# Optimization experiments

Hardware: AMD Instinct MI355X
Metric: run time of the kernel (lower is better)

## Reference

```python
import jax, jax.numpy as jnp
import numpy as np

N_NODES = 50000
N_EDGES = 500000
F_DIM = 128
N_REL = 8
N_LAYERS = 2
NEG_SLOPE = 0.2  # PyG RGATConv default negative_slope


def setup_inputs() -> dict:
    key = jax.random.key(0)
    ks = jax.random.split(key, 6)
    x = jax.random.normal(ks[0], (N_NODES, F_DIM), dtype=jnp.float32)
    edge_index = jax.random.randint(ks[1], (2, N_EDGES), 0, N_NODES)
    edge_type = jax.random.randint(ks[2], (N_EDGES,), 0, N_REL)
    # Per-layer relation weights [L, R, F_in, F_out], attention vectors q,k [L, F_out, 1], bias [L, F_out]
    W = jax.random.normal(ks[3], (N_LAYERS, N_REL, F_DIM, F_DIM), dtype=jnp.float32) * (1.0 / np.sqrt(F_DIM)).astype(np.float32)
    att_q = jax.random.normal(ks[4], (N_LAYERS, F_DIM, 1), dtype=jnp.float32) * 0.1
    att_k = jax.random.normal(ks[5], (N_LAYERS, F_DIM, 1), dtype=jnp.float32) * 0.1
    bias = jnp.zeros((N_LAYERS, F_DIM), dtype=jnp.float32)
    return {"x": x, "W": W, "att_q": att_q, "att_k": att_k, "bias": bias,
            "edge_index": edge_index, "edge_type": edge_type}


def _segment_softmax(logits, seg, num_segments):
    # Numerically stable softmax over edges grouped by destination node.
    m = jax.ops.segment_max(logits, seg, num_segments=num_segments)
    m = jax.lax.stop_gradient(m)
    e = jnp.exp(logits - m[seg])
    denom = jax.ops.segment_sum(e, seg, num_segments=num_segments)
    return e / (denom[seg] + 1e-16)


def _rgat_layer(h, src, dst, edge_type, W, q, k, b):
    # h: [N, F]; W: [R, F, F]. Project once per relation, then gather per edge
    # (avoids materializing [E, F, F] per-edge weight gathers).
    n = h.shape[0]
    xw = jnp.einsum('nf,rfg->rng', h, W)          # [R, N, F]
    out_j = xw[edge_type, src]                    # [E, F] transformed source feats
    out_i = xw[edge_type, dst]                    # [E, F] transformed dest feats
    # additive self-attention: leaky_relu(q(x_i) + k(x_j)), heads=1, dim=1
    logits = jax.nn.leaky_relu((out_i @ q + out_j @ k)[:, 0], NEG_SLOPE)  # [E]
    alpha = _segment_softmax(logits, dst, n)      # across-relation softmax per dst node
    agg = jax.ops.segment_sum(alpha[:, None] * out_j, dst, num_segments=n)  # [N, F]
    return agg + b


def reference(x, W, att_q, att_k, bias, edge_index, edge_type):
    src, dst = edge_index[0], edge_index[1]
    h = x
    for l in range(W.shape[0]):  # small fixed layer count
        h = _rgat_layer(h, src, dst, edge_type, W[l], att_q[l], att_k[l], bias[l])
        h = jax.nn.relu(h)  # dropout is identity in eval mode
    return h
```

## Files before the change

kernel.cpp:

```cpp
#include <hip/hip_runtime.h>
#include <hip/hip_bf16.h>
#include <hip/hip_fp16.h>

#define N_NODES 50000
#define N_EDGES 500000
#define F_DIM   128
#define N_REL   8
#define N_LAYERS 2
#define NEG_SLOPE 0.2f

#define NBLK_N ((N_NODES + 255) / 256)

typedef _Float16 half8 __attribute__((ext_vector_type(8)));
typedef float f32x4  __attribute__((ext_vector_type(4)));


__device__ inline float lrelu(float l) { return (l > 0.f) ? l : NEG_SLOPE * l; }

__global__ __launch_bounds__(256) void prep_h(const float* __restrict__ H,
                                              _Float16* __restrict__ Hf) {
    const size_t i8 = (size_t)blockIdx.x * 256 + threadIdx.x;
    if (i8 >= (size_t)N_NODES * F_DIM / 8) return;
    const float* src = H + i8 * 8;
    float av[8];
    *(float4*)(av)     = *(const float4*)(src);
    *(float4*)(av + 4) = *(const float4*)(src + 4);
    alignas(16) _Float16 hb[8];
#pragma unroll
    for (int j = 0; j < 8; ++j) hb[j] = (_Float16)av[j];
    *(uint4*)(Hf + i8 * 8) = *(const uint4*)hb;
}

__global__ __launch_bounds__(256) void prep_w(const float* __restrict__ W,
                                              _Float16* __restrict__ Wf) {
    __shared__ float tile[64][F_DIM + 1];
    const int mat = blockIdx.x;
    const float* src = W + (size_t)mat * F_DIM * F_DIM;
    const int t = threadIdx.x;
    for (int hf = 0; hf < 2; ++hf) {
#pragma unroll
        for (int i = 0; i < 8; ++i) {
            int idx = t + i * 256;
            int f = idx >> 5, c4 = idx & 31;
            float4 v = *(const float4*)(src + (size_t)(hf * 64 + f) * F_DIM + c4 * 4);
            *(float4*)&tile[f][c4 * 4] = v;
        }
        __syncthreads();
        int g = t >> 1, fs = (t & 1) * 32;
        for (int c = 0; c < 4; ++c) {
            alignas(16) _Float16 th[8];
#pragma unroll
            for (int j = 0; j < 8; ++j) th[j] = (_Float16)tile[fs + c * 8 + j][g];
            size_t o = ((size_t)mat * F_DIM + g) * F_DIM + hf * 64 + fs + c * 8;
            *(uint4*)(Wf + o) = *(const uint4*)th;
        }
        __syncthreads();
    }
}

#define GBM 512
__global__ __launch_bounds__(256, 2) void gemm_xw(const _Float16* __restrict__ Hf,
                                                  const _Float16* __restrict__ Wf,
                                                  const float* __restrict__ qv_g,
                                                  const float* __restrict__ kv_g,
                                                  __half* __restrict__ xw,
                                                  float* __restrict__ a_q,
                                                  float* __restrict__ a_k) {
    __shared__ _Float16 lds[F_DIM * F_DIM];
    const int r   = blockIdx.y;
    const int tid = threadIdx.x;
    const int lane = tid & 63, w = tid >> 6;
    const int q = lane >> 4, ln = lane & 15;

    {
        const _Float16* src = Wf + (size_t)r * F_DIM * F_DIM;
#pragma unroll
        for (int i = 0; i < 8; ++i) {
            int chunk = tid + i * 256;
            int gg = chunk >> 4, c8 = chunk & 15;
            uint4 v = *(const uint4*)(src + gg * F_DIM + c8 * 8);
            *(uint4*)(lds + gg * F_DIM + ((c8 ^ (gg & 15)) * 8)) = v;
        }
    }

    float qvl[8], kvl[8];
#pragma unroll
    for (int t = 0; t < 8; ++t) {
        qvl[t] = qv_g[t * 16 + ln];
        kvl[t] = kv_g[t * 16 + ln];
    }

    __syncthreads();

    for (int t4 = 0; t4 < 4; ++t4) {
        const int rb0 = blockIdx.x * GBM + t4 * 128;
        if (rb0 >= N_NODES) break;

        half8 Af[2][4];
#pragma unroll
        for (int rt = 0; rt < 2; ++rt) {
            int row = rb0 + w * 32 + rt * 16 + ln;
            int ar = (row < N_NODES) ? row : (N_NODES - 1);
            const _Float16* hp = Hf + (size_t)ar * F_DIM;
#pragma unroll
            for (int ks = 0; ks < 4; ++ks)
                Af[rt][ks] = *(const half8*)(hp + ks * 32 + q * 8);
        }

        f32x4 acc[2][8];
#pragma unroll
        for (int rt = 0; rt < 2; ++rt)
#pragma unroll
            for (int t = 0; t < 8; ++t) acc[rt][t] = (f32x4)(0.f);

#pragma unroll
        for (int ks = 0; ks < 4; ++ks) {
            const int jx = (((ks * 4 + q) ^ ln)) << 3;
            half8 Bf[8];
#pragma unroll
            for (int c = 0; c < 8; ++c)
                Bf[c] = *(const half8*)(lds + (c * 16 + ln) * F_DIM + jx);
#pragma unroll
            for (int c = 0; c < 8; ++c)
#pragma unroll
                for (int rt = 0; rt < 2; ++rt)
                    acc[rt][c] = __builtin_amdgcn_mfma_f32_16x16x32_f16(Af[rt][ks], Bf[c], acc[rt][c], 0, 0, 0);
        }

#pragma unroll
        for (int rt = 0; rt < 2; ++rt) {
            float pq[4], pk[4];
#pragma unroll
            for (int reg = 0; reg < 4; ++reg) {
                const int row = rb0 + w * 32 + rt * 16 + q * 4 + reg;
                alignas(16) unsigned short hs[8];
                float sq = 0.f, sk = 0.f;
#pragma unroll
                for (int t = 0; t < 8; ++t) {
                    float v = acc[rt][t][reg];
                    __half hv = __float2half(v);
                    hs[t] = *reinterpret_cast<unsigned short*>(&hv);
                    sq = fmaf(v, qvl[t], sq);
                    sk = fmaf(v, kvl[t], sk);
                }
                if (row < N_NODES)
                    *(uint4*)(xw + ((size_t)r * N_NODES + row) * F_DIM + ln * 8) = *(const uint4*)hs;
                pq[reg] = sq; pk[reg] = sk;
            }
#pragma unroll
            for (int reg = 0; reg < 4; ++reg) {
#pragma unroll
                for (int m = 1; m <= 8; m <<= 1) {
                    pq[reg] += __shfl_xor(pq[reg], m);
                    pk[reg] += __shfl_xor(pk[reg], m);
                }
            }
            if (ln == 0) {
#pragma unroll
                for (int reg = 0; reg < 4; ++reg) {
                    const int row = rb0 + w * 32 + rt * 16 + q * 4 + reg;
                    if (row < N_NODES) {
                        a_q[r * N_NODES + row] = pq[reg];
                        a_k[r * N_NODES + row] = pk[reg];
                    }
                }
            }
        }
    }
}


__global__ __launch_bounds__(256) void count_kernel(const int* __restrict__ dstp,
                                                    int* __restrict__ cnt) {
    int e = blockIdx.x * 256 + threadIdx.x;
    if (e < N_EDGES) atomicAdd(cnt + dstp[e], 1);
}

__global__ __launch_bounds__(256) void block_sum_kernel(const int* __restrict__ cnt,
                                                        int* __restrict__ partial) {
    __shared__ int s[256];
    int idx = blockIdx.x * 256 + threadIdx.x;
    int v = (idx < N_NODES) ? cnt[idx] : 0;
    s[threadIdx.x] = v;
    __syncthreads();
    for (int off = 128; off > 0; off >>= 1) {
        if (threadIdx.x < off) s[threadIdx.x] += s[threadIdx.x + off];
        __syncthreads();
    }
    if (threadIdx.x == 0) partial[blockIdx.x] = s[0];
}

__global__ __launch_bounds__(256) void scan_partials_kernel(int* __restrict__ partial,
                                                            int* __restrict__ row_ptr) {
    __shared__ int s[256];
    int t = threadIdx.x;
    int v = (t < NBLK_N) ? partial[t] : 0;
    s[t] = v;
    __syncthreads();
#pragma unroll
    for (int off = 1; off < 256; off <<= 1) {
        int x = (t >= off) ? s[t - off] : 0;
        __syncthreads();
        s[t] += x;
        __syncthreads();
    }
    if (t < NBLK_N) partial[t] = s[t] - v;
    if (t == 0) row_ptr[N_NODES] = N_EDGES;
}

__global__ __launch_bounds__(256) void scan_block_kernel(const int* __restrict__ cnt,
                                                         const int* __restrict__ partial,
                                                         int* __restrict__ row_ptr) {
    __shared__ int s[256];
    int t = threadIdx.x;
    int idx = blockIdx.x * 256 + t;
    int v = (idx < N_NODES) ? cnt[idx] : 0;
    s[t] = v;
    __syncthreads();
#pragma unroll
    for (int off = 1; off < 256; off <<= 1) {
        int x = (t >= off) ? s[t - off] : 0;
        __syncthreads();
        s[t] += x;
        __syncthreads();
    }
    if (idx < N_NODES) row_ptr[idx] = partial[blockIdx.x] + s[t] - v;
}

__global__ __launch_bounds__(256) void scatter_kernel(const int* __restrict__ srcp,
                                                      const int* __restrict__ dstp,
                                                      const int* __restrict__ etp,
                                                      const int* __restrict__ row_ptr,
                                                      int* __restrict__ cursor,
                                                      unsigned* __restrict__ sorted,
                                                      unsigned short* __restrict__ dst16) {
    int e = blockIdx.x * 256 + threadIdx.x;
    if (e >= N_EDGES) return;
    int d = dstp[e];
    int pos = atomicAdd(cursor + d, 1);
    int j = row_ptr[d] + pos;
    sorted[j] = (unsigned)srcp[e] | ((unsigned)etp[e] << 16);
    dst16[j] = (unsigned short)d;
}

__global__ __launch_bounds__(256) void logits_kernel(const float* __restrict__ a_q,
                                                     const float* __restrict__ a_k,
                                                     const unsigned* __restrict__ sorted,
                                                     const unsigned short* __restrict__ dst16,
                                                     float* __restrict__ lgt) {
    int j = blockIdx.x * 256 + threadIdx.x;
    if (j >= N_EDGES) return;
    unsigned p = sorted[j];
    int s = p & 0xffff, t = p >> 16;
    int d = dst16[j];
    lgt[j] = lrelu(a_q[t * N_NODES + d] + a_k[t * N_NODES + s]);
}

__device__ inline void accum8(float* acc, uint4 v, float a) {
    const __half2* h2 = reinterpret_cast<const __half2*>(&v);
#pragma unroll
    for (int t = 0; t < 4; ++t) {
        float2 f = __half22float2(h2[t]);
        acc[t * 2]     = fmaf(a, f.x, acc[t * 2]);
        acc[t * 2 + 1] = fmaf(a, f.y, acc[t * 2 + 1]);
    }
}
__device__ inline const uint4* xwrow(const __half* xw, unsigned p, int ln) {
    return (const uint4*)(xw + (((size_t)(p >> 16)) * N_NODES + (p & 0xffff)) * F_DIM + ln * 8);
}

__global__ __launch_bounds__(256) void agg_fused(const __half* __restrict__ xw,
                                                 const float* __restrict__ lgt,
                                                 const int* __restrict__ row_ptr,
                                                 const unsigned* __restrict__ sorted,
                                                 const float* __restrict__ bias,
                                                 float* __restrict__ outp,
                                                 _Float16* __restrict__ hfp) {
    const int lane = threadIdx.x & 63;
    const int wave = threadIdx.x >> 6;
    const int half = lane >> 5, hl = lane & 31;
    const int d0 = blockIdx.x * 8 + wave * 2;
    if (d0 >= N_NODES) return;
    const int dmy = d0 + half;
    const int dv = (dmy < N_NODES) ? dmy : (N_NODES - 1);
    const int beg = row_ptr[dv], end = row_ptr[dv + 1];
    int cnt = (dmy < N_NODES) ? (end - beg) : 0;
    const int cntO = __shfl_xor(cnt, 32);
    const int cmax = (cnt > cntO) ? cnt : cntO;

    if (cmax <= 32) {
        unsigned p = 0;
        float l = -3.4e38f;
        if (hl < cnt) {
            p = sorted[beg + hl];
            l = lgt[beg + hl];
        }
        float m = l;
#pragma unroll
        for (int off = 16; off > 0; off >>= 1) m = fmaxf(m, __shfl_xor(m, off, 32));
        const float ex = (hl < cnt) ? __expf(l - m) : 0.f;

        const int gg = hl >> 4, ln = hl & 15;
        float acc[8] = {0, 0, 0, 0, 0, 0, 0, 0};
        for (int i = 0; i < cnt; i += 4) {
            unsigned p0 = __shfl(p, i + gg, 32);
            unsigned p1 = __shfl(p, i + 2 + gg, 32);
            float a0 = __shfl(ex, i + gg, 32);
            float a1 = __shfl(ex, i + 2 + gg, 32);
            uint4 v0 = *xwrow(xw, p0, ln);
            uint4 v1 = *xwrow(xw, p1, ln);
            accum8(acc, v0, a0);
            accum8(acc, v1, a1);
        }
        float dsum = ex;
#pragma unroll
        for (int off = 16; off > 0; off >>= 1) dsum += __shfl_xor(dsum, off, 32);
#pragma unroll
        for (int t = 0; t < 8; ++t) acc[t] += __shfl_xor(acc[t], 16, 32);

        if (dmy < N_NODES) {
            const float inv = 1.f / (dsum + 1e-16f);
#pragma unroll
            for (int j = 0; j < 4; ++j) {
                const int t = gg * 4 + j;
                const int col = t * 16 + ln;
                const float v = fmaxf(fmaf(acc[t], inv, bias[col]), 0.f);
                if (outp) outp[(size_t)dmy * F_DIM + col] = v;
                if (hfp)  hfp[(size_t)dmy * F_DIM + col] = (_Float16)v;
            }
        }
    } else {
        const int g = lane >> 4, ln = lane & 15;
        for (int h = 0; h < 2; ++h) {
            const int dd = d0 + h;
            if (dd >= N_NODES) continue;
            const int b = __shfl(beg, h * 32);
            const int c = __shfl(cnt, h * 32);
            if (c <= 64) {
                unsigned p = 0;
                float l = -3.4e38f;
                if (lane < c) {
                    p = sorted[b + lane];
                    l = lgt[b + lane];
                }
                float m = l;
#pragma unroll
                for (int off = 32; off > 0; off >>= 1) m = fmaxf(m, __shfl_xor(m, off));
                const float ex = (lane < c) ? __expf(l - m) : 0.f;
                float acc[8] = {0, 0, 0, 0, 0, 0, 0, 0};
                for (int i = 0; i < c; i += 8) {
                    unsigned p0 = __shfl(p, i + g);
                    unsigned p1 = __shfl(p, i + 4 + g);
                    float a0 = __shfl(ex, i + g);
                    float a1 = __shfl(ex, i + 4 + g);
                    uint4 v0 = *xwrow(xw, p0, ln);
                    uint4 v1 = *xwrow(xw, p1, ln);
                    accum8(acc, v0, a0);
                    accum8(acc, v1, a1);
                }
                float dsum = ex;
#pragma unroll
                for (int off = 32; off > 0; off >>= 1) dsum += __shfl_xor(dsum, off);
#pragma unroll
                for (int t = 0; t < 8; ++t) {
                    acc[t] += __shfl_xor(acc[t], 16);
                    acc[t] += __shfl_xor(acc[t], 32);
                }
                const float inv = 1.f / (dsum + 1e-16f);
#pragma unroll
                for (int j = 0; j < 2; ++j) {
                    const int t = g * 2 + j;
                    const int col = t * 16 + ln;
                    const float v = fmaxf(fmaf(acc[t], inv, bias[col]), 0.f);
                    if (outp) outp[(size_t)dd * F_DIM + col] = v;
                    if (hfp)  hfp[(size_t)dd * F_DIM + col] = (_Float16)v;
                }
            } else {
                const int p0 = lane * 2;
                const int c0 = (p0 & 7) * 16 + (p0 >> 3);
                const int c1 = c0 + 16;
                float2 acc = make_float2(bias[c0], bias[c1]);
                float m = -3.4e38f;
                for (int i = b + lane; i < b + c; i += 64) m = fmaxf(m, lgt[i]);
#pragma unroll
                for (int off = 32; off > 0; off >>= 1) m = fmaxf(m, __shfl_xor(m, off));
                float dsum = 0.f;
                for (int i = b + lane; i < b + c; i += 64) dsum += __expf(lgt[i] - m);
#pragma unroll
                for (int off = 32; off > 0; off >>= 1) dsum += __shfl_xor(dsum, off);
                const float inv = 1.f / (dsum + 1e-16f);
                for (int i = b; i < b + c; ++i) {
                    unsigned pp = sorted[i];
                    float alpha = __expf(lgt[i] - m) * inv;
                    const __half2 h2 = *((const __half2*)xw + (((size_t)(pp >> 16)) * N_NODES + (pp & 0xffff)) * (F_DIM / 2) + lane);
                    float2 v = make_float2(__half2float(h2.x), __half2float(h2.y));
                    acc.x = fmaf(alpha, v.x, acc.x);
                    acc.y = fmaf(alpha, v.y, acc.y);
                }
                const float v0 = fmaxf(acc.x, 0.f), v1 = fmaxf(acc.y, 0.f);
                if (outp) { outp[(size_t)dd * F_DIM + c0] = v0; outp[(size_t)dd * F_DIM + c1] = v1; }
                if (hfp)  { hfp[(size_t)dd * F_DIM + c0] = (_Float16)v0; hfp[(size_t)dd * F_DIM + c1] = (_Float16)v1; }
            }
        }
    }
}


extern "C" void kernel_launch(void* const* d_in, const int* in_sizes, int n_in,
                              void* d_out, int out_size, void* d_ws, size_t ws_size,
                              hipStream_t stream) {
    const float* x     = (const float*)d_in[0];
    const float* W     = (const float*)d_in[1];
    const float* att_q = (const float*)d_in[2];
    const float* att_k = (const float*)d_in[3];
    const float* bias  = (const float*)d_in[4];
    const int* ei      = (const int*)d_in[5];
    const int* etp     = (const int*)d_in[6];
    const int* srcp = ei;
    const int* dstp = ei + N_EDGES;
    float* out = (float*)d_out;
    char* ws   = (char*)d_ws;

    size_t off = 0;
    auto alloc = [&](size_t bytes) {
        void* p = ws + off;
        off = (off + bytes + 511) & ~(size_t)511;
        return p;
    };
    __half* xw       = (__half*)alloc((size_t)N_REL * N_NODES * F_DIM * sizeof(__half));
    float* a_q       = (float*)alloc((size_t)N_REL * N_NODES * sizeof(float));
    float* a_k       = (float*)alloc((size_t)N_REL * N_NODES * sizeof(float));
    int* cnt         = (int*)alloc((size_t)2 * N_NODES * sizeof(int));
    int* cursor      = cnt + N_NODES;
    int* row_ptr     = (int*)alloc(((size_t)N_NODES + 1) * sizeof(int));
    int* partial     = (int*)alloc(256 * sizeof(int));
    unsigned* sorted = (unsigned*)alloc((size_t)N_EDGES * sizeof(unsigned));
    unsigned short* dst16 = (unsigned short*)alloc((size_t)N_EDGES * sizeof(unsigned short));
    float* lgt       = (float*)alloc((size_t)N_EDGES * sizeof(float));
    _Float16* Wf     = (_Float16*)alloc((size_t)N_LAYERS * N_REL * F_DIM * F_DIM * sizeof(_Float16));
    _Float16* Hf     = (_Float16*)alloc((size_t)N_NODES * F_DIM * sizeof(_Float16));

    prep_w<<<N_LAYERS * N_REL, 256, 0, stream>>>(W, Wf);
    hipMemsetAsync(cnt, 0, (size_t)2 * N_NODES * 4, stream);
    count_kernel<<<(N_EDGES + 255) / 256, 256, 0, stream>>>(dstp, cnt);
    block_sum_kernel<<<NBLK_N, 256, 0, stream>>>(cnt, partial);
    scan_partials_kernel<<<1, 256, 0, stream>>>(partial, row_ptr);
    scan_block_kernel<<<NBLK_N, 256, 0, stream>>>(cnt, partial, row_ptr);
    scatter_kernel<<<(N_EDGES + 255) / 256, 256, 0, stream>>>(
        srcp, dstp, etp, row_ptr, cursor, sorted, dst16);

    const int grid_h = (N_NODES * F_DIM / 8 + 255) / 256;
    const int grid_m = (N_NODES + GBM - 1) / GBM;
    const int grid_e = (N_EDGES + 255) / 256;
    prep_h<<<grid_h, 256, 0, stream>>>(x, Hf);
    for (int l = 0; l < N_LAYERS; ++l) {
        gemm_xw<<<dim3(grid_m, N_REL), 256, 0, stream>>>(
            Hf, Wf + (size_t)l * N_REL * F_DIM * F_DIM,
            att_q + l * F_DIM, att_k + l * F_DIM,
            xw, a_q, a_k);
        logits_kernel<<<grid_e, 256, 0, stream>>>(a_q, a_k, sorted, dst16, lgt);
        const bool last = (l == N_LAYERS - 1);
        agg_fused<<<(N_NODES + 7) / 8, 256, 0, stream>>>(
            xw, lgt, row_ptr, sorted, bias + l * F_DIM,
            last ? out : nullptr,
            last ? nullptr : Hf);
    }
}
```

Measured before the change: 291.6 us.

## Precompute W·q/W·k vectors, compute attention scores via separate MFMA kernel, drop softmax max

Folds the attention vectors into the relation weights ahead of time (W_r·q, W_r·k) and computes the per-node attention scalars with a small MFMA kernel. This takes the dot-product and shuffle reductions out of the main projection GEMM epilogue. It also removes the per-destination max subtraction in the softmax, and unrolls the gather loop to four rows per step. The cost is an extra kernel launch plus a reread of H, and skipping the max subtraction risks exp overflow for large logits.

Measured after the change: 301.3 us. 1.03x slower.

```diff
diff --git a/kernel.cpp b/kernel.cpp
--- a/kernel.cpp
+++ b/kernel.cpp
@@ -58,14 +58,56 @@
     }
 }
 
+__global__ __launch_bounds__(256) void prep_vqk(const float* __restrict__ W,
+                                                const float* __restrict__ att_q,
+                                                const float* __restrict__ att_k,
+                                                _Float16* __restrict__ vb) {
+    const int l = blockIdx.x >> 3, r = blockIdx.x & 7;
+    __shared__ float qk[2 * F_DIM];
+    const int t = threadIdx.x;
+    qk[t] = (t < F_DIM) ? att_q[l * F_DIM + t] : att_k[l * F_DIM + (t - F_DIM)];
+    __syncthreads();
+    const float* Wr = W + ((size_t)(l * N_REL + r)) * F_DIM * F_DIM;
+    const int f = t & (F_DIM - 1);
+    const float* qv = (t < F_DIM) ? qk : qk + F_DIM;
+    float s = 0.f;
+    for (int g = 0; g < F_DIM; g += 4) {
+        float4 wv = *(const float4*)(Wr + (size_t)f * F_DIM + g);
+        s += wv.x * qv[g] + wv.y * qv[g + 1] + wv.z * qv[g + 2] + wv.w * qv[g + 3];
+    }
+    const int c = (t < F_DIM) ? r : (N_REL + r);
+    vb[((size_t)l * 16 + c) * F_DIM + f] = (_Float16)s;
+}
+
+__global__ __launch_bounds__(256) void aqk_kernel(const _Float16* __restrict__ Hf,
+                                                  const _Float16* __restrict__ vbl,
+                                                  float* __restrict__ a_q,
+                                                  float* __restrict__ a_k) {
+    const int w = threadIdx.x >> 6, lane = threadIdx.x & 63;
+    const int q = lane >> 4, ln = lane & 15;
+    const int row0 = blockIdx.x * 64 + w * 16;
+    f32x4 acc = (f32x4)(0.f);
+#pragma unroll
+    for (int ks = 0; ks < 4; ++ks) {
+        int rr = row0 + ln; if (rr >= N_NODES) rr = N_NODES - 1;
+        half8 af = *(const half8*)(Hf + (size_t)rr * F_DIM + ks * 32 + q * 8);
+        half8 bf = *(const half8*)(vbl + (size_t)ln * F_DIM + ks * 32 + q * 8);
+        acc = __builtin_amdgcn_mfma_f32_16x16x32_f16(af, bf, acc, 0, 0, 0);
+    }
+#pragma unroll
+    for (int reg = 0; reg < 4; ++reg) {
+        const int row = row0 + q * 4 + reg;
+        if (row < N_NODES) {
+            if (ln < N_REL) a_q[ln * N_NODES + row] = acc[reg];
+            else            a_k[(ln - N_REL) * N_NODES + row] = acc[reg];
+        }
+    }
+}
+
 #define GBM 512
 __global__ __launch_bounds__(256, 2) void gemm_xw(const _Float16* __restrict__ Hf,
                                                   const _Float16* __restrict__ Wf,
-                                                  const float* __restrict__ qv_g,
-                                                  const float* __restrict__ kv_g,
-                                                  __half* __restrict__ xw,
-                                                  float* __restrict__ a_q,
-                                                  float* __restrict__ a_k) {
+                                                  __half* __restrict__ xw) {
     __shared__ _Float16 lds[F_DIM * F_DIM];
     const int r   = blockIdx.y;
     const int tid = threadIdx.x;
@@ -83,13 +125,6 @@
         }
     }
 
-    float qvl[8], kvl[8];
-#pragma unroll
-    for (int t = 0; t < 8; ++t) {
-        qvl[t] = qv_g[t * 16 + ln];
-        kvl[t] = kv_g[t * 16 + ln];
-    }
-
     __syncthreads();
 
     for (int t4 = 0; t4 < 4; ++t4) {
@@ -129,41 +164,17 @@
 
 #pragma unroll
         for (int rt = 0; rt < 2; ++rt) {
-            float pq[4], pk[4];
 #pragma unroll
             for (int reg = 0; reg < 4; ++reg) {
                 const int row = rb0 + w * 32 + rt * 16 + q * 4 + reg;
                 alignas(16) unsigned short hs[8];
-                float sq = 0.f, sk = 0.f;
 #pragma unroll
                 for (int t = 0; t < 8; ++t) {
-                    float v = acc[rt][t][reg];
-                    __half hv = __float2half(v);
+                    __half hv = __float2half(acc[rt][t][reg]);
                     hs[t] = *reinterpret_cast<unsigned short*>(&hv);
-                    sq = fmaf(v, qvl[t], sq);
-                    sk = fmaf(v, kvl[t], sk);
                 }
                 if (row < N_NODES)
                     *(uint4*)(xw + ((size_t)r * N_NODES + row) * F_DIM + ln * 8) = *(const uint4*)hs;
-                pq[reg] = sq; pk[reg] = sk;
-            }
-#pragma unroll
-            for (int reg = 0; reg < 4; ++reg) {
-#pragma unroll
-                for (int m = 1; m <= 8; m <<= 1) {
-                    pq[reg] += __shfl_xor(pq[reg], m);
-                    pk[reg] += __shfl_xor(pk[reg], m);
-                }
-            }
-            if (ln == 0) {
-#pragma unroll
-                for (int reg = 0; reg < 4; ++reg) {
-                    const int row = rb0 + w * 32 + rt * 16 + q * 4 + reg;
-                    if (row < N_NODES) {
-                        a_q[r * N_NODES + row] = pq[reg];
-                        a_k[r * N_NODES + row] = pk[reg];
-                    }
-                }
             }
         }
     }
@@ -290,27 +301,31 @@
 
     if (cmax <= 32) {
         unsigned p = 0;
-        float l = -3.4e38f;
+        float ex = 0.f;
         if (hl < cnt) {
             p = sorted[beg + hl];
-            l = lgt[beg + hl];
-        }
-        float m = l;
-#pragma unroll
-        for (int off = 16; off > 0; off >>= 1) m = fmaxf(m, __shfl_xor(m, off, 32));
-        const float ex = (hl < cnt) ? __expf(l - m) : 0.f;
+            ex = __expf(lgt[beg + hl]);
+        }
 
         const int gg = hl >> 4, ln = hl & 15;
         float acc[8] = {0, 0, 0, 0, 0, 0, 0, 0};
-        for (int i = 0; i < cnt; i += 4) {
+        for (int i = 0; i < cnt; i += 8) {
             unsigned p0 = __shfl(p, i + gg, 32);
             unsigned p1 = __shfl(p, i + 2 + gg, 32);
+            unsigned p2 = __shfl(p, i + 4 + gg, 32);
+            unsigned p3 = __shfl(p, i + 6 + gg, 32);
             float a0 = __shfl(ex, i + gg, 32);
             float a1 = __shfl(ex, i + 2 + gg, 32);
+            float a2 = __shfl(ex, i + 4 + gg, 32);
+            float a3 = __shfl(ex, i + 6 + gg, 32);
             uint4 v0 = *xwrow(xw, p0, ln);
             uint4 v1 = *xwrow(xw, p1, ln);
+            uint4 v2 = *xwrow(xw, p2, ln);
+            uint4 v3 = *xwrow(xw, p3, ln);
             accum8(acc, v0, a0);
             accum8(acc, v1, a1);
+            accum8(acc, v2, a2);
+            accum8(acc, v3, a3);
         }
         float dsum = ex;
 #pragma unroll
@@ -438,9 +453,11 @@
     unsigned short* dst16 = (unsigned short*)alloc((size_t)N_EDGES * sizeof(unsigned short));
     float* lgt       = (float*)alloc((size_t)N_EDGES * sizeof(float));
     _Float16* Wf     = (_Float16*)alloc((size_t)N_LAYERS * N_REL * F_DIM * F_DIM * sizeof(_Float16));
+    _Float16* vb     = (_Float16*)alloc((size_t)N_LAYERS * 16 * F_DIM * sizeof(_Float16));
     _Float16* Hf     = (_Float16*)alloc((size_t)N_NODES * F_DIM * sizeof(_Float16));
 
     prep_w<<<N_LAYERS * N_REL, 256, 0, stream>>>(W, Wf);
+    prep_vqk<<<N_LAYERS * N_REL, 256, 0, stream>>>(W, att_q, att_k, vb);
     hipMemsetAsync(cnt, 0, (size_t)2 * N_NODES * 4, stream);
     count_kernel<<<(N_EDGES + 255) / 256, 256, 0, stream>>>(dstp, cnt);
     block_sum_kernel<<<NBLK_N, 256, 0, stream>>>(cnt, partial);
@@ -452,12 +469,12 @@
     const int grid_h = (N_NODES * F_DIM / 8 + 255) / 256;
     const int grid_m = (N_NODES + GBM - 1) / GBM;
     const int grid_e = (N_EDGES + 255) / 256;
+    const int grid_a = (N_NODES + 63) / 64;
     prep_h<<<grid_h, 256, 0, stream>>>(x, Hf);
     for (int l = 0; l < N_LAYERS; ++l) {
         gemm_xw<<<dim3(grid_m, N_REL), 256, 0, stream>>>(
-            Hf, Wf + (size_t)l * N_REL * F_DIM * F_DIM,
-            att_q + l * F_DIM, att_k + l * F_DIM,
-            xw, a_q, a_k);
+            Hf, Wf + (size_t)l * N_REL * F_DIM * F_DIM, xw);
+        aqk_kernel<<<grid_a, 256, 0, stream>>>(Hf, vb + (size_t)l * 16 * F_DIM, a_q, a_k);
         logits_kernel<<<grid_e, 256, 0, stream>>>(a_q, a_k, sorted, dst16, lgt);
         const bool last = (l == N_LAYERS - 1);
         agg_fused<<<(N_NODES + 7) / 8, 256, 0, stream>>>(
```

## Aggregate four destination nodes per wave and drop softmax max subtraction

Applied to the files above, without the earlier changes.

Aggregation now assigns 16 lanes to each destination node, so a wave handles four nodes instead of two; each lane covers all eight feature slices. The inner loop issues four gathered row loads per iteration instead of two. The per-node max reduction before the exponent is removed, exponentiating raw logits directly. This aims to improve lane use and memory-level parallelism for low-degree nodes. In exchange, waves holding any node with more than 16 edges fall back to a serial four-node slow path, and the softmax can overflow if logits are large.

Result: no change. 294.6 us (+1.0%).

```diff
diff --git a/kernel.cpp b/kernel.cpp
--- a/kernel.cpp
+++ b/kernel.cpp
@@ -278,52 +278,52 @@
                                                  _Float16* __restrict__ hfp) {
     const int lane = threadIdx.x & 63;
     const int wave = threadIdx.x >> 6;
-    const int half = lane >> 5, hl = lane & 31;
-    const int d0 = blockIdx.x * 8 + wave * 2;
+    const int ql = lane & 15;
+    const int d0 = blockIdx.x * 16 + wave * 4;
     if (d0 >= N_NODES) return;
-    const int dmy = d0 + half;
+    const int dmy = d0 + (lane >> 4);
     const int dv = (dmy < N_NODES) ? dmy : (N_NODES - 1);
     const int beg = row_ptr[dv], end = row_ptr[dv + 1];
-    int cnt = (dmy < N_NODES) ? (end - beg) : 0;
-    const int cntO = __shfl_xor(cnt, 32);
-    const int cmax = (cnt > cntO) ? cnt : cntO;
-
-    if (cmax <= 32) {
+    const int cnt = (dmy < N_NODES) ? (end - beg) : 0;
+    int cmax = cnt;
+    cmax = max(cmax, __shfl_xor(cmax, 16));
+    cmax = max(cmax, __shfl_xor(cmax, 32));
+
+    if (cmax <= 16) {
         unsigned p = 0;
-        float l = -3.4e38f;
-        if (hl < cnt) {
-            p = sorted[beg + hl];
-            l = lgt[beg + hl];
-        }
-        float m = l;
-#pragma unroll
-        for (int off = 16; off > 0; off >>= 1) m = fmaxf(m, __shfl_xor(m, off, 32));
-        const float ex = (hl < cnt) ? __expf(l - m) : 0.f;
-
-        const int gg = hl >> 4, ln = hl & 15;
+        float ex = 0.f;
+        if (ql < cnt) {
+            p = sorted[beg + ql];
+            ex = __expf(lgt[beg + ql]);
+        }
         float acc[8] = {0, 0, 0, 0, 0, 0, 0, 0};
         for (int i = 0; i < cnt; i += 4) {
-            unsigned p0 = __shfl(p, i + gg, 32);
-            unsigned p1 = __shfl(p, i + 2 + gg, 32);
-            float a0 = __shfl(ex, i + gg, 32);
-            float a1 = __shfl(ex, i + 2 + gg, 32);
-            uint4 v0 = *xwrow(xw, p0, ln);
-            uint4 v1 = *xwrow(xw, p1, ln);
+            unsigned p0 = __shfl(p, i, 16);
+            unsigned p1 = __shfl(p, i + 1, 16);
+            unsigned p2 = __shfl(p, i + 2, 16);
+            unsigned p3 = __shfl(p, i + 3, 16);
+            float a0 = __shfl(ex, i, 16);
+            float a1 = __shfl(ex, i + 1, 16);
+            float a2 = __shfl(ex, i + 2, 16);
+            float a3 = __shfl(ex, i + 3, 16);
+            uint4 v0 = *xwrow(xw, p0, ql);
+            uint4 v1 = *xwrow(xw, p1, ql);
+            uint4 v2 = *xwrow(xw, p2, ql);
+            uint4 v3 = *xwrow(xw, p3, ql);
             accum8(acc, v0, a0);
             accum8(acc, v1, a1);
+            accum8(acc, v2, a2);
+            accum8(acc, v3, a3);
         }
         float dsum = ex;
 #pragma unroll
-        for (int off = 16; off > 0; off >>= 1) dsum += __shfl_xor(dsum, off, 32);
-#pragma unroll
-        for (int t = 0; t < 8; ++t) acc[t] += __shfl_xor(acc[t], 16, 32);
+        for (int off = 8; off > 0; off >>= 1) dsum += __shfl_xor(dsum, off, 16);
 
         if (dmy < N_NODES) {
             const float inv = 1.f / (dsum + 1e-16f);
 #pragma unroll
-            for (int j = 0; j < 4; ++j) {
-                const int t = gg * 4 + j;
-                const int col = t * 16 + ln;
+            for (int t = 0; t < 8; ++t) {
+                const int col = t * 16 + ql;
                 const float v = fmaxf(fmaf(acc[t], inv, bias[col]), 0.f);
                 if (outp) outp[(size_t)dmy * F_DIM + col] = v;
                 if (hfp)  hfp[(size_t)dmy * F_DIM + col] = (_Float16)v;
@@ -331,11 +331,11 @@
         }
     } else {
         const int g = lane >> 4, ln = lane & 15;
-        for (int h = 0; h < 2; ++h) {
+        for (int h = 0; h < 4; ++h) {
             const int dd = d0 + h;
             if (dd >= N_NODES) continue;
-            const int b = __shfl(beg, h * 32);
-            const int c = __shfl(cnt, h * 32);
+            const int b = __shfl(beg, h * 16);
+            const int c = __shfl(cnt, h * 16);
             if (c <= 64) {
                 unsigned p = 0;
                 float l = -3.4e38f;
@@ -460,7 +460,7 @@
             xw, a_q, a_k);
         logits_kernel<<<grid_e, 256, 0, stream>>>(a_q, a_k, sorted, dst16, lgt);
         const bool last = (l == N_LAYERS - 1);
-        agg_fused<<<(N_NODES + 7) / 8, 256, 0, stream>>>(
+        agg_fused<<<(N_NODES + 15) / 16, 256, 0, stream>>>(
             xw, lgt, row_ptr, sorted, bias + l * F_DIM,
             last ? out : nullptr,
             last ? nullptr : Hf);
```
